# Optimization experiments

Hardware: AMD Instinct MI355X
Metric: run time of the kernel (lower is better)

## Reference

```python
import jax, jax.numpy as jnp
import numpy as np

CODEBOOK_DIM = 8
CODEBOOK_SIZE = 8192
INPUT_DIM = 1024
B, T = 8, 2048


def setup_inputs() -> dict:
    key = jax.random.key(0)
    ks = jax.random.split(key, 6)
    z = jax.random.normal(ks[0], (B, INPUT_DIM, T), dtype=jnp.float32)
    # weight_norm(Conv1d(k=1)) is a reparameterization; effective weight is a dense matrix
    W_in = jax.random.normal(ks[1], (CODEBOOK_DIM, INPUT_DIM), dtype=jnp.float32) * 0.03
    b_in = jax.random.normal(ks[2], (CODEBOOK_DIM,), dtype=jnp.float32) * 0.01
    W_out = jax.random.normal(ks[3], (INPUT_DIM, CODEBOOK_DIM), dtype=jnp.float32) * 0.1
    b_out = jax.random.normal(ks[4], (INPUT_DIM,), dtype=jnp.float32) * 0.01
    codebook = jax.random.normal(ks[5], (CODEBOOK_SIZE, CODEBOOK_DIM), dtype=jnp.float32)
    return {"z": z, "W_in": W_in, "b_in": b_in, "W_out": W_out, "b_out": b_out,
            "codebook": codebook}


def _l2norm(x, axis=-1, eps=1e-12):
    # matches torch F.normalize: x / max(||x||, eps)
    n = jnp.sqrt(jnp.sum(x * x, axis=axis, keepdims=True))
    return x / jnp.maximum(n, eps)


def reference(z, W_in, b_in, W_out, b_out, codebook):
    # in-project: 1x1 conv == matmul over channel dim. z_e: [B, 8, T]
    z_e = jnp.einsum('dc,bct->bdt', W_in, z) + b_in[None, :, None]

    # decode latents: flatten to [B*T, 8], normalize both sides
    enc = z_e.transpose(0, 2, 1).reshape(-1, CODEBOOK_DIM)
    enc_n = _l2norm(enc)
    cb_n = _l2norm(codebook)
    dist = (jnp.sum(enc_n * enc_n, axis=1, keepdims=True)
            - 2.0 * enc_n @ cb_n.T
            + jnp.sum(cb_n * cb_n, axis=1)[None, :])  # [B*T, 8192]
    indices = jnp.argmax(-dist, axis=1).reshape(B, T)  # [B, T]

    # gather UNnormalized codebook vectors, back to [B, 8, T]
    z_q = codebook[indices].transpose(0, 2, 1)

    # straight-through estimator
    z_q = z_e + jax.lax.stop_gradient(z_q - z_e)

    # out-project
    out = jnp.einsum('cd,bdt->bct', W_out, z_q) + b_out[None, :, None]
    return out, indices, z_e
```

## Files before the change

kernel.cpp:

```cpp
#include <hip/hip_runtime.h>
#include <float.h>

#define B_   8
#define T_   2048
#define CIN  1024
#define DD   8
#define KC   8192
#define NTOK (B_*T_)
#define NSLICE 16
#define SLICE (KC/NSLICE)

#define IDX_OFF ((size_t)B_*CIN*T_)
#define ZE_OFF  (IDX_OFF + NTOK)

#define WS_ENCN  0
#define WS_SE    (WS_ENCN + NTOK*DD)
#define WS_PDIST (WS_SE + NTOK)
#define WS_PIDX  (WS_PDIST + NSLICE*NTOK)

__device__ __forceinline__ int wskew(int c) { return (c << 3) + (((c >> 6) & 7) << 2); }

__global__ __launch_bounds__(256) void inproj(const float* __restrict__ z,
                                              const float* __restrict__ W_in,
                                              const float* __restrict__ b_in,
                                              float* __restrict__ out,
                                              float* __restrict__ ws) {
    __shared__ float wt[CIN * DD];
    __shared__ float red[8][32][DD];
    int tid = threadIdx.x;
    for (int idx = tid; idx < CIN * DD; idx += 256) {
        int d = idx >> 10, c = idx & 1023;
        wt[c * 8 + d] = W_in[idx];
    }
    __syncthreads();

    int bid = blockIdx.x;
    int b  = bid >> 6;
    int tg = bid & 63;
    int t0 = tg * 32;
    int g = tid >> 5, tl = tid & 31;

    const float* zp = z + ((size_t)b * CIN) * T_ + (t0 + tl);
    float acc[8] = {0, 0, 0, 0, 0, 0, 0, 0};
    int cbeg = g * 128;
    #pragma unroll 8
    for (int c = cbeg; c < cbeg + 128; ++c) {
        float v = zp[(size_t)c * T_];
        const float4* w4 = (const float4*)&wt[c * DD];
        float4 w0 = w4[0], w1 = w4[1];
        acc[0] = fmaf(w0.x, v, acc[0]);
        acc[1] = fmaf(w0.y, v, acc[1]);
        acc[2] = fmaf(w0.z, v, acc[2]);
        acc[3] = fmaf(w0.w, v, acc[3]);
        acc[4] = fmaf(w1.x, v, acc[4]);
        acc[5] = fmaf(w1.y, v, acc[5]);
        acc[6] = fmaf(w1.z, v, acc[6]);
        acc[7] = fmaf(w1.w, v, acc[7]);
    }
    #pragma unroll
    for (int d = 0; d < 8; ++d) red[g][tl][d] = acc[d];
    __syncthreads();

    if (tid < 32) {
        int tt = tid;
        float ze[8];
        #pragma unroll
        for (int d = 0; d < 8; ++d) {
            float s01 = (red[0][tt][d] + red[1][tt][d]) + (red[2][tt][d] + red[3][tt][d]);
            float s23 = (red[4][tt][d] + red[5][tt][d]) + (red[6][tt][d] + red[7][tt][d]);
            ze[d] = (s01 + s23) + b_in[d];
        }
        float* zeo = out + ZE_OFF + ((size_t)b * DD) * T_ + (t0 + tt);
        #pragma unroll
        for (int d = 0; d < 8; ++d) zeo[(size_t)d * T_] = ze[d];
        float s2 = __fmul_rn(ze[0], ze[0]);
        #pragma unroll
        for (int d = 1; d < 8; ++d) s2 = __fadd_rn(s2, __fmul_rn(ze[d], ze[d]));
        float m = fmaxf(sqrtf(s2), 1e-12f);
        float en[8];
        #pragma unroll
        for (int d = 0; d < 8; ++d) en[d] = ze[d] / m;
        float se = __fmul_rn(en[0], en[0]);
        #pragma unroll
        for (int d = 1; d < 8; ++d) se = __fadd_rn(se, __fmul_rn(en[d], en[d]));
        int token = b * T_ + t0 + tt;
        float4* ep = (float4*)(ws + WS_ENCN + (size_t)token * DD);
        ep[0] = make_float4(en[0], en[1], en[2], en[3]);
        ep[1] = make_float4(en[4], en[5], en[6], en[7]);
        ws[WS_SE + token] = se;
    }
}

__global__ __launch_bounds__(256) void vq_search(const float* __restrict__ cb,
                                                 float* __restrict__ ws) {
    __shared__ float lcb[SLICE * DD];
    __shared__ float lsc[SLICE];
    int tid = threadIdx.x;
    int bid = blockIdx.x;
    int sl = bid & (NSLICE - 1);
    int tg = bid >> 4;

    #pragma unroll
    for (int r = 0; r < 2; ++r) {
        int jl = tid + r * 256;
        const float4* src = (const float4*)(cb + (size_t)(sl * SLICE + jl) * DD);
        float4 a = src[0], bv = src[1];
        float c[8] = {a.x, a.y, a.z, a.w, bv.x, bv.y, bv.z, bv.w};
        float s2 = __fmul_rn(c[0], c[0]);
        #pragma unroll
        for (int k = 1; k < 8; ++k) s2 = __fadd_rn(s2, __fmul_rn(c[k], c[k]));
        float m = fmaxf(sqrtf(s2), 1e-12f);
        float cn[8];
        #pragma unroll
        for (int k = 0; k < 8; ++k) cn[k] = c[k] / m;
        float sc = __fmul_rn(cn[0], cn[0]);
        #pragma unroll
        for (int k = 1; k < 8; ++k) sc = __fadd_rn(sc, __fmul_rn(cn[k], cn[k]));
        float4* dst = (float4*)&lcb[jl * DD];
        dst[0] = make_float4(cn[0], cn[1], cn[2], cn[3]);
        dst[1] = make_float4(cn[4], cn[5], cn[6], cn[7]);
        lsc[jl] = sc;
    }
    __syncthreads();

    int token0 = tg * 512 + tid * 2;
    float e[2][8], se[2];
    #pragma unroll
    for (int m = 0; m < 2; ++m) {
        const float4* ep = (const float4*)(ws + WS_ENCN + (size_t)(token0 + m) * DD);
        float4 a = ep[0], bv = ep[1];
        e[m][0] = a.x;  e[m][1] = a.y;  e[m][2] = a.z;  e[m][3] = a.w;
        e[m][4] = bv.x; e[m][5] = bv.y; e[m][6] = bv.z; e[m][7] = bv.w;
        se[m] = ws[WS_SE + token0 + m];
    }

    float best[2] = {FLT_MAX, FLT_MAX};
    int bi[2] = {0, 0};
    #pragma unroll 4
    for (int j = 0; j < SLICE; ++j) {
        float4 ca = *(const float4*)&lcb[j * 8];
        float4 cbv = *(const float4*)&lcb[j * 8 + 4];
        float sc = lsc[j];
        float cd[8] = {ca.x, ca.y, ca.z, ca.w, cbv.x, cbv.y, cbv.z, cbv.w};
        #pragma unroll
        for (int m = 0; m < 2; ++m) {
            float dot = e[m][0] * cd[0];
            #pragma unroll
            for (int k = 1; k < 8; ++k) dot = fmaf(e[m][k], cd[k], dot);
            float dist = __fadd_rn(fmaf(-2.f, dot, se[m]), sc);
            bool p = dist < best[m];
            best[m] = p ? dist : best[m];
            bi[m]   = p ? j : bi[m];
        }
    }
    *(float2*)(ws + WS_PDIST + (size_t)sl * NTOK + token0) = make_float2(best[0], best[1]);
    *(int2*)((int*)ws + WS_PIDX + (size_t)sl * NTOK + token0) =
        make_int2(sl * SLICE + bi[0], sl * SLICE + bi[1]);
}

__global__ __launch_bounds__(256) void outproj(const float* __restrict__ ws,
                                               const float* __restrict__ cb,
                                               const float* __restrict__ W_out,
                                               const float* __restrict__ b_out,
                                               float* __restrict__ out) {
    __shared__ float wo[8224];
    __shared__ float bo[1032];
    __shared__ float zql[DD * 64];
    int tid = threadIdx.x;
    for (int i = tid; i < CIN * DD; i += 256) {
        int c = i >> 3, d = i & 7;
        wo[wskew(c) + d] = W_out[i];
    }
    for (int i = tid; i < CIN; i += 256) bo[i + ((i >> 6) & 7)] = b_out[i];

    int bid = blockIdx.x;
    int b = bid >> 5, tg = bid & 31;
    int t0 = tg * 64;

    if (tid < 64) {
        int tl = tid;
        int token = b * T_ + t0 + tl;
        float bestv = ws[WS_PDIST + token];
        int bi = ((const int*)ws)[WS_PIDX + token];
        #pragma unroll
        for (int s = 1; s < NSLICE; ++s) {
            float d = ws[WS_PDIST + (size_t)s * NTOK + token];
            int i2  = ((const int*)ws)[WS_PIDX + (size_t)s * NTOK + token];
            bool p = d < bestv;
            bestv = p ? d : bestv;
            bi    = p ? i2 : bi;
        }
        out[IDX_OFF + token] = (float)bi;
        const float* zep = out + ZE_OFF + ((size_t)b * DD) * T_ + (t0 + tl);
        float4 ca = *(const float4*)(cb + (size_t)bi * DD);
        float4 cb2 = *(const float4*)(cb + (size_t)bi * DD + 4);
        float cv[8] = {ca.x, ca.y, ca.z, ca.w, cb2.x, cb2.y, cb2.z, cb2.w};
        #pragma unroll
        for (int d = 0; d < 8; ++d) {
            float ze = zep[(size_t)d * T_];
            zql[d * 64 + tl] = __fadd_rn(ze, __fsub_rn(cv[d], ze));
        }
    }
    __syncthreads();

    int qi = tid & 15, g = tid >> 4;
    float q[4][8];
    #pragma unroll
    for (int m = 0; m < 4; ++m)
        #pragma unroll
        for (int k = 0; k < 8; ++k) q[m][k] = zql[k * 64 + qi * 4 + m];

    float* op = out + ((size_t)b * CIN) * T_ + t0 + qi * 4;
    int cbeg = g * 64;
    int bskew = (g & 7);
    #pragma unroll 4
    for (int i = 0; i < 64; ++i) {
        int c = cbeg + i;
        int w0 = wskew(c);
        float4 wa = *(const float4*)&wo[w0];
        float4 wb = *(const float4*)&wo[w0 + 4];
        float wd[8] = {wa.x, wa.y, wa.z, wa.w, wb.x, wb.y, wb.z, wb.w};
        float bc = bo[c + bskew];
        float r[4];
        #pragma unroll
        for (int m = 0; m < 4; ++m) {
            float dot = q[m][0] * wd[0];
            #pragma unroll
            for (int k = 1; k < 8; ++k) dot = fmaf(q[m][k], wd[k], dot);
            r[m] = dot + bc;
        }
        *(float4*)(op + (size_t)c * T_) = make_float4(r[0], r[1], r[2], r[3]);
    }
}

extern "C" void kernel_launch(void* const* d_in, const int* in_sizes, int n_in,
                              void* d_out, int out_size, void* d_ws, size_t ws_size,
                              hipStream_t stream) {
    const float* z     = (const float*)d_in[0];
    const float* W_in  = (const float*)d_in[1];
    const float* b_in  = (const float*)d_in[2];
    const float* W_out = (const float*)d_in[3];
    const float* b_out = (const float*)d_in[4];
    const float* cb    = (const float*)d_in[5];
    float* out = (float*)d_out;
    float* ws  = (float*)d_ws;

    inproj<<<NTOK / 32, 256, 0, stream>>>(z, W_in, b_in, out, ws);
    vq_search<<<(NTOK / 512) * NSLICE, 256, 0, stream>>>(cb, ws);
    outproj<<<NTOK / 64, 256, 0, stream>>>(ws, cb, W_out, b_out, out);
}
```

Before: 194.0 us.

## Precompute normalized codebook and transposed weights in prep kernel, read via scalar loads

Adds a prep kernel that normalizes the codebook and transposes W_in once into workspace. The inproj, vq_search and outproj kernels drop their per-block LDS staging and instead read weights and codebook entries with wave-uniform (scalar/constant-cache) loads, using readfirstlane to make the group index uniform. The search slices are doubled to 32 for more blocks. outproj now uses 512 threads with one token per thread and scalar W_out reads. This removes redundant per-block normalization and LDS fills, at the cost of an extra launch and reliance on the scalar cache.

```diff
diff --git a/kernel.cpp b/kernel.cpp
--- a/kernel.cpp
+++ b/kernel.cpp
@@ -7,61 +7,85 @@
 #define DD   8
 #define KC   8192
 #define NTOK (B_*T_)
-#define NSLICE 16
+#define NSLICE 32
 #define SLICE (KC/NSLICE)
 
 #define IDX_OFF ((size_t)B_*CIN*T_)
 #define ZE_OFF  (IDX_OFF + NTOK)
 
-#define WS_ENCN  0
+#define WS_WT    0
+#define WS_CBN   (WS_WT + CIN*DD)
+#define WS_SC    (WS_CBN + KC*DD)
+#define WS_ENCN  (WS_SC + KC)
 #define WS_SE    (WS_ENCN + NTOK*DD)
 #define WS_PDIST (WS_SE + NTOK)
 #define WS_PIDX  (WS_PDIST + NSLICE*NTOK)
 
-__device__ __forceinline__ int wskew(int c) { return (c << 3) + (((c >> 6) & 7) << 2); }
-
-__global__ __launch_bounds__(256) void inproj(const float* __restrict__ z,
-                                              const float* __restrict__ W_in,
+__global__ __launch_bounds__(256) void prep(const float* __restrict__ cb,
+                                            const float* __restrict__ W_in,
+                                            float* __restrict__ ws) {
+    int gt = blockIdx.x * 256 + threadIdx.x;
+    if (gt < KC) {
+        const float4* src = (const float4*)(cb + (size_t)gt * DD);
+        float4 a = src[0], bv = src[1];
+        float c[8] = {a.x, a.y, a.z, a.w, bv.x, bv.y, bv.z, bv.w};
+        float s2 = __fmul_rn(c[0], c[0]);
+        #pragma unroll
+        for (int k = 1; k < 8; ++k) s2 = __fadd_rn(s2, __fmul_rn(c[k], c[k]));
+        float m = fmaxf(sqrtf(s2), 1e-12f);
+        float cn[8];
+        #pragma unroll
+        for (int k = 0; k < 8; ++k) cn[k] = c[k] / m;
+        float sc = __fmul_rn(cn[0], cn[0]);
+        #pragma unroll
+        for (int k = 1; k < 8; ++k) sc = __fadd_rn(sc, __fmul_rn(cn[k], cn[k]));
+        float4* dst = (float4*)(ws + WS_CBN + (size_t)gt * DD);
+        dst[0] = make_float4(cn[0], cn[1], cn[2], cn[3]);
+        dst[1] = make_float4(cn[4], cn[5], cn[6], cn[7]);
+        ws[WS_SC + gt] = sc;
+    } else if (gt < KC + CIN * DD) {
+        int i = gt - KC;
+        int c = i >> 3, d = i & 7;
+        ws[WS_WT + i] = W_in[d * CIN + c];
+    }
+}
+
+__global__ __launch_bounds__(512) void inproj(const float* __restrict__ z,
                                               const float* __restrict__ b_in,
                                               float* __restrict__ out,
                                               float* __restrict__ ws) {
-    __shared__ float wt[CIN * DD];
-    __shared__ float red[8][32][DD];
+    __shared__ float red[8][64][9];
     int tid = threadIdx.x;
-    for (int idx = tid; idx < CIN * DD; idx += 256) {
-        int d = idx >> 10, c = idx & 1023;
-        wt[c * 8 + d] = W_in[idx];
-    }
-    __syncthreads();
+    int g = __builtin_amdgcn_readfirstlane(tid >> 6);
+    int tl = tid & 63;
 
     int bid = blockIdx.x;
-    int b  = bid >> 6;
-    int tg = bid & 63;
-    int t0 = tg * 32;
-    int g = tid >> 5, tl = tid & 31;
+    int b = bid >> 5, tg = bid & 31;
+    int t0 = tg * 64;
 
     const float* zp = z + ((size_t)b * CIN) * T_ + (t0 + tl);
+    const float* wt = ws + WS_WT;
     float acc[8] = {0, 0, 0, 0, 0, 0, 0, 0};
     int cbeg = g * 128;
     #pragma unroll 8
-    for (int c = cbeg; c < cbeg + 128; ++c) {
+    for (int i = 0; i < 128; ++i) {
+        int c = cbeg + i;
         float v = zp[(size_t)c * T_];
-        const float4* w4 = (const float4*)&wt[c * DD];
-        float4 w0 = w4[0], w1 = w4[1];
-        acc[0] = fmaf(w0.x, v, acc[0]);
-        acc[1] = fmaf(w0.y, v, acc[1]);
-        acc[2] = fmaf(w0.z, v, acc[2]);
-        acc[3] = fmaf(w0.w, v, acc[3]);
-        acc[4] = fmaf(w1.x, v, acc[4]);
-        acc[5] = fmaf(w1.y, v, acc[5]);
-        acc[6] = fmaf(w1.z, v, acc[6]);
-        acc[7] = fmaf(w1.w, v, acc[7]);
+        const float* w = wt + c * 8;
+        acc[0] = fmaf(w[0], v, acc[0]);
+        acc[1] = fmaf(w[1], v, acc[1]);
+        acc[2] = fmaf(w[2], v, acc[2]);
+        acc[3] = fmaf(w[3], v, acc[3]);
+        acc[4] = fmaf(w[4], v, acc[4]);
+        acc[5] = fmaf(w[5], v, acc[5]);
+        acc[6] = fmaf(w[6], v, acc[6]);
+        acc[7] = fmaf(w[7], v, acc[7]);
     }
     #pragma unroll
     for (int d = 0; d < 8; ++d) red[g][tl][d] = acc[d];
     __syncthreads();
 
-    if (tid < 32) {
+    if (tid < 64) {
         int tt = tid;
         float ze[8];
         #pragma unroll
@@ -91,37 +115,11 @@
     }
 }
 
-__global__ __launch_bounds__(256) void vq_search(const float* __restrict__ cb,
-                                                 float* __restrict__ ws) {
-    __shared__ float lcb[SLICE * DD];
-    __shared__ float lsc[SLICE];
+__global__ __launch_bounds__(256) void vq_search(float* __restrict__ ws) {
     int tid = threadIdx.x;
     int bid = blockIdx.x;
     int sl = bid & (NSLICE - 1);
-    int tg = bid >> 4;
-
-    #pragma unroll
-    for (int r = 0; r < 2; ++r) {
-        int jl = tid + r * 256;
-        const float4* src = (const float4*)(cb + (size_t)(sl * SLICE + jl) * DD);
-        float4 a = src[0], bv = src[1];
-        float c[8] = {a.x, a.y, a.z, a.w, bv.x, bv.y, bv.z, bv.w};
-        float s2 = __fmul_rn(c[0], c[0]);
-        #pragma unroll
-        for (int k = 1; k < 8; ++k) s2 = __fadd_rn(s2, __fmul_rn(c[k], c[k]));
-        float m = fmaxf(sqrtf(s2), 1e-12f);
-        float cn[8];
-        #pragma unroll
-        for (int k = 0; k < 8; ++k) cn[k] = c[k] / m;
-        float sc = __fmul_rn(cn[0], cn[0]);
-        #pragma unroll
-        for (int k = 1; k < 8; ++k) sc = __fadd_rn(sc, __fmul_rn(cn[k], cn[k]));
-        float4* dst = (float4*)&lcb[jl * DD];
-        dst[0] = make_float4(cn[0], cn[1], cn[2], cn[3]);
-        dst[1] = make_float4(cn[4], cn[5], cn[6], cn[7]);
-        lsc[jl] = sc;
-    }
-    __syncthreads();
+    int tg = bid >> 5;
 
     int token0 = tg * 512 + tid * 2;
     float e[2][8], se[2];
@@ -134,14 +132,15 @@
         se[m] = ws[WS_SE + token0 + m];
     }
 
+    const float* cbn = ws + WS_CBN + (size_t)sl * SLICE * DD;
+    const float* csc = ws + WS_SC + sl * SLICE;
+
     float best[2] = {FLT_MAX, FLT_MAX};
     int bi[2] = {0, 0};
     #pragma unroll 4
     for (int j = 0; j < SLICE; ++j) {
-        float4 ca = *(const float4*)&lcb[j * 8];
-        float4 cbv = *(const float4*)&lcb[j * 8 + 4];
-        float sc = lsc[j];
-        float cd[8] = {ca.x, ca.y, ca.z, ca.w, cbv.x, cbv.y, cbv.z, cbv.w};
+        const float* cd = cbn + j * 8;
+        float sc = csc[j];
         #pragma unroll
         for (int m = 0; m < 2; ++m) {
             float dot = e[m][0] * cd[0];
@@ -158,27 +157,21 @@
         make_int2(sl * SLICE + bi[0], sl * SLICE + bi[1]);
 }
 
-__global__ __launch_bounds__(256) void outproj(const float* __restrict__ ws,
+__global__ __launch_bounds__(512) void outproj(const float* __restrict__ ws,
                                                const float* __restrict__ cb,
                                                const float* __restrict__ W_out,
                                                const float* __restrict__ b_out,
                                                float* __restrict__ out) {
-    __shared__ float wo[8224];
-    __shared__ float bo[1032];
     __shared__ float zql[DD * 64];
     int tid = threadIdx.x;
-    for (int i = tid; i < CIN * DD; i += 256) {
-        int c = i >> 3, d = i & 7;
-        wo[wskew(c) + d] = W_out[i];
-    }
-    for (int i = tid; i < CIN; i += 256) bo[i + ((i >> 6) & 7)] = b_out[i];
+    int g = __builtin_amdgcn_readfirstlane(tid >> 6);
+    int tl = tid & 63;
 
     int bid = blockIdx.x;
     int b = bid >> 5, tg = bid & 31;
     int t0 = tg * 64;
 
     if (tid < 64) {
-        int tl = tid;
         int token = b * T_ + t0 + tl;
         float bestv = ws[WS_PDIST + token];
         int bi = ((const int*)ws)[WS_PIDX + token];
@@ -203,33 +196,26 @@
     }
     __syncthreads();
 
-    int qi = tid & 15, g = tid >> 4;
-    float q[4][8];
+    float q[8];
     #pragma unroll
-    for (int m = 0; m < 4; ++m)
-        #pragma unroll
-        for (int k = 0; k < 8; ++k) q[m][k] = zql[k * 64 + qi * 4 + m];
-
-    float* op = out + ((size_t)b * CIN) * T_ + t0 + qi * 4;
-    int cbeg = g * 64;
-    int bskew = (g & 7);
-    #pragma unroll 4
-    for (int i = 0; i < 64; ++i) {
+    for (int k = 0; k < 8; ++k) q[k] = zql[k * 64 + tl];
+
+    float* op = out + ((size_t)b * CIN) * T_ + t0 + tl;
+    int cbeg = g * 128;
+    #pragma unroll 8
+    for (int i = 0; i < 128; ++i) {
         int c = cbeg + i;
-        int w0 = wskew(c);
-        float4 wa = *(const float4*)&wo[w0];
-        float4 wb = *(const float4*)&wo[w0 + 4];
-        float wd[8] = {wa.x, wa.y, wa.z, wa.w, wb.x, wb.y, wb.z, wb.w};
-        float bc = bo[c + bskew];
-        float r[4];
-        #pragma unroll
-        for (int m = 0; m < 4; ++m) {
-            float dot = q[m][0] * wd[0];
-            #pragma unroll
-            for (int k = 1; k < 8; ++k) dot = fmaf(q[m][k], wd[k], dot);
-            r[m] = dot + bc;
-        }
-        *(float4*)(op + (size_t)c * T_) = make_float4(r[0], r[1], r[2], r[3]);
+        const float* w = W_out + (size_t)c * 8;
+        float bc = b_out[c];
+        float dot = q[0] * w[0];
+        dot = fmaf(q[1], w[1], dot);
+        dot = fmaf(q[2], w[2], dot);
+        dot = fmaf(q[3], w[3], dot);
+        dot = fmaf(q[4], w[4], dot);
+        dot = fmaf(q[5], w[5], dot);
+        dot = fmaf(q[6], w[6], dot);
+        dot = fmaf(q[7], w[7], dot);
+        op[(size_t)c * T_] = dot + bc;
     }
 }
 
@@ -245,7 +231,8 @@
     float* out = (float*)d_out;
     float* ws  = (float*)d_ws;
 
-    inproj<<<NTOK / 32, 256, 0, stream>>>(z, W_in, b_in, out, ws);
-    vq_search<<<(NTOK / 512) * NSLICE, 256, 0, stream>>>(cb, ws);
-    outproj<<<NTOK / 64, 256, 0, stream>>>(ws, cb, W_out, b_out, out);
-}
+    prep<<<64, 256, 0, stream>>>(cb, W_in, ws);
+    inproj<<<NTOK / 64, 512, 0, stream>>>(z, b_in, out, ws);
+    vq_search<<<(NTOK / 512) * NSLICE, 256, 0, stream>>>(ws);
+    outproj<<<NTOK / 64, 512, 0, stream>>>(ws, cb, W_out, b_out, out);
+}
```

Result: slower. 202.7 us (+4.4%).
